# Kernel optimization log

Hardware: AMD Instinct MI355X
Metric: run time of the kernel (lower is better)

## Reference

```python
import jax, jax.numpy as jnp
import numpy as np

N_FFT = 512
N_STAGES = 4
BASE = N_FFT >> N_STAGES          # base DFT size = 32
SPLIT0 = N_FFT // 2 + 1           # rfft bins = 257
BATCH = 32768


def _mod_seq(order):
    # bit-reversed offset sequence used by get_partial_bit_reversal_matrix
    mset = [0]
    for o in range(order):
        step = 2 ** o
        mset = [v for x in mset for v in (x, x + step)]
    return mset


def _perm_indices():
    # gather indices equivalent to the partial bit-reversal permutation matmul
    base = 2 ** N_STAGES
    n_per = N_FFT // base
    idx = []
    for p in _mod_seq(N_STAGES):
        idx.extend(j * base + p for j in range(n_per))
    return np.asarray(idx, dtype=np.int32)

_PERM_IDX = _perm_indices()
_DFT = np.fft.fft(np.eye(BASE))   # symmetric DFT matrix, M[j,k]=exp(-2pi i jk/BASE)


def setup_inputs() -> dict:
    key = jax.random.key(0)
    x = jax.random.normal(key, (BATCH, N_FFT), dtype=jnp.float32)
    return {"x": x}


def reference(x):
    dt = x.dtype
    dft_r = jnp.asarray(_DFT.real, dtype=dt)
    dft_i = jnp.asarray(_DFT.imag, dtype=dt)

    B = x.shape[0]
    # partial bit-reversal permutation (FFTPermuter) as a gather
    y = x[..., _PERM_IDX].reshape(B, 2 ** N_STAGES, BASE)
    ev = y[:, ::2]   # even-decimated sub-sequences (B, 2^(s-1), BASE)
    od = y[:, 1::2]  # odd-decimated  sub-sequences

    # base-case DFT (DFT module): x @ M with symmetric M
    ev_r = jnp.einsum('bml,lk->bmk', ev, dft_r)
    ev_i = jnp.einsum('bml,lk->bmk', ev, dft_i)
    od_r = jnp.einsum('bml,lk->bmk', od, dft_r)
    od_i = jnp.einsum('bml,lk->bmk', od, dft_i)

    # radix-2 butterfly combine stages (FFTwiddle with SIMPLE ops)
    L = BASE
    for _ in range(N_STAGES):
        w = np.exp(-2j * np.pi * np.arange(L) / (2 * L))
        tw_r = jnp.asarray(w.real, dtype=dt)
        tw_i = jnp.asarray(w.imag, dtype=dt)
        todd_r = tw_r * od_r - tw_i * od_i
        todd_i = tw_r * od_i + tw_i * od_r
        real = jnp.concatenate([ev_r + todd_r, ev_r - todd_r], axis=-1)
        imag = jnp.concatenate([ev_i + todd_i, ev_i - todd_i], axis=-1)
        ev_r, od_r = real[:, ::2], real[:, 1::2]
        ev_i, od_i = imag[:, ::2], imag[:, 1::2]
        L *= 2

    # rfft truncation (torch.split in _RFFTDecompWithGMAC)
    yre = ev_r[:, 0, :SPLIT0]
    yim = ev_i[:, 0, :SPLIT0]
    return (yre, yim)
```

## Files before the change

kernel.cpp:

```cpp
#include <hip/hip_runtime.h>


#define NFFT 512
#define WPB  4

__device__ __forceinline__ int SW(int i) { return i ^ ((i >> 2) & 12); }

__device__ __forceinline__ void waveSyncLds() {
    asm volatile("s_waitcnt lgkmcnt(0)" ::: "memory");
}

__global__ __launch_bounds__(256) void rfft512_kernel(
    const float* __restrict__ x, float* __restrict__ out, int batch)
{
    __shared__ __align__(16) float2 lds[WPB][2][256];
    const int t = threadIdx.x & 63;
    const int w = threadIdx.x >> 6;
    long long b = (long long)blockIdx.x * WPB + w;
    if (b >= batch) b = batch - 1;

    float2* buf0 = lds[w][0];
    float2* buf1 = lds[w][1];
    const float NEG2PI = -6.28318530717958647692f;
    const float C45 = 0.70710678118654752440f;

    {
        const float2* xf2 = (const float2*)(x + b * NFFT);
        float2 a  = xf2[t];
        float2 bb = xf2[t + 64];
        float2 c  = xf2[t + 128];
        float2 d  = xf2[t + 192];
        float apcr = a.x + c.x, apci = a.y + c.y;
        float amcr = a.x - c.x, amci = a.y - c.y;
        float bpdr = bb.x + d.x, bpdi = bb.y + d.y;
        float bmdr = bb.x - d.x, bmdi = bb.y - d.y;
        float y0r = apcr + bpdr, y0i = apci + bpdi;
        float u1r = amcr + bmdi, u1i = amci - bmdr;
        float u2r = apcr - bpdr, u2i = apci - bpdi;
        float u3r = amcr - bmdi, u3i = amci + bmdr;
        float sn, cs;
        __sincosf(NEG2PI * (float)t * (1.0f / 256.0f), &sn, &cs);
        float w1r = cs, w1i = sn;
        float w2r = cs * cs - sn * sn, w2i = 2.0f * cs * sn;
        float w3r = w1r * w2r - w1i * w2i, w3i = w1r * w2i + w1i * w2r;
        int wb = (4 * t) ^ (t & 12);
        float4* d4 = (float4*)buf1;
        d4[wb >> 1]       = make_float4(y0r, y0i,
                                        w1r * u1r - w1i * u1i, w1r * u1i + w1i * u1r);
        d4[(wb >> 1) + 1] = make_float4(w2r * u2r - w2i * u2i, w2r * u2i + w2i * u2r,
                                        w3r * u3r - w3i * u3i, w3r * u3i + w3i * u3r);
    }
    waveSyncLds();

    {
        int rb = SW(t);
        float2 a = buf1[rb], bb = buf1[rb + 64], c = buf1[rb + 128], d = buf1[rb + 192];
        float apcr = a.x + c.x, apci = a.y + c.y;
        float amcr = a.x - c.x, amci = a.y - c.y;
        float bpdr = bb.x + d.x, bpdi = bb.y + d.y;
        float bmdr = bb.x - d.x, bmdi = bb.y - d.y;
        float y0r = apcr + bpdr, y0i = apci + bpdi;
        float u1r = amcr + bmdi, u1i = amci - bmdr;
        float u2r = apcr - bpdr, u2i = apci - bpdi;
        float u3r = amcr - bmdi, u3i = amci + bmdr;
        float sn, cs;
        __sincosf(NEG2PI * (float)(t >> 2) * (1.0f / 64.0f), &sn, &cs);
        float w1r = cs, w1i = sn;
        float w2r = cs * cs - sn * sn, w2i = 2.0f * cs * sn;
        float w3r = w1r * w2r - w1i * w2i, w3i = w1r * w2i + w1i * w2r;
        int wbase = (t & 3) + 16 * (t >> 2);
        buf0[SW(wbase)]      = make_float2(y0r, y0i);
        buf0[SW(wbase + 4)]  = make_float2(w1r * u1r - w1i * u1i, w1r * u1i + w1i * u1r);
        buf0[SW(wbase + 8)]  = make_float2(w2r * u2r - w2i * u2i, w2r * u2i + w2i * u2r);
        buf0[SW(wbase + 12)] = make_float2(w3r * u3r - w3i * u3i, w3r * u3i + w3i * u3r);
    }
    waveSyncLds();

    {
        int rb = SW(t);
        float2 a = buf0[rb], bb = buf0[rb + 64], c = buf0[rb + 128], d = buf0[rb + 192];
        float apcr = a.x + c.x, apci = a.y + c.y;
        float amcr = a.x - c.x, amci = a.y - c.y;
        float bpdr = bb.x + d.x, bpdi = bb.y + d.y;
        float bmdr = bb.x - d.x, bmdi = bb.y - d.y;
        float y0r = apcr + bpdr, y0i = apci + bpdi;
        float u1r = amcr + bmdi, u1i = amci - bmdr;
        float u2r = apcr - bpdr, u2i = apci - bpdi;
        float u3r = amcr - bmdi, u3i = amci + bmdr;
        float sn, cs;
        __sincosf(NEG2PI * (float)(t >> 4) * (1.0f / 16.0f), &sn, &cs);
        float w1r = cs, w1i = sn;
        float w2r = cs * cs - sn * sn, w2i = 2.0f * cs * sn;
        float w3r = w1r * w2r - w1i * w2i, w3i = w1r * w2i + w1i * w2r;
        int wbase = (t & 15) + 64 * (t >> 4);
        buf1[SW(wbase)]      = make_float2(y0r, y0i);
        buf1[SW(wbase + 16)] = make_float2(w1r * u1r - w1i * u1i, w1r * u1i + w1i * u1r);
        buf1[SW(wbase + 32)] = make_float2(w2r * u2r - w2i * u2i, w2r * u2i + w2i * u2r);
        buf1[SW(wbase + 48)] = make_float2(w3r * u3r - w3i * u3i, w3r * u3i + w3i * u3r);
    }
    waveSyncLds();

    float zr[4], zi[4];
    {
        int rb = SW(t);
        float2 a = buf1[rb], bb = buf1[rb + 64], c = buf1[rb + 128], d = buf1[rb + 192];
        float apcr = a.x + c.x, apci = a.y + c.y;
        float amcr = a.x - c.x, amci = a.y - c.y;
        float bpdr = bb.x + d.x, bpdi = bb.y + d.y;
        float bmdr = bb.x - d.x, bmdi = bb.y - d.y;
        zr[0] = apcr + bpdr; zi[0] = apci + bpdi;
        zr[1] = amcr + bmdi; zi[1] = amci - bmdr;
        zr[2] = apcr - bpdr; zi[2] = apci - bpdi;
        zr[3] = amcr - bmdi; zi[3] = amci + bmdr;
        buf0[rb]       = make_float2(zr[0], zi[0]);
        buf0[rb + 64]  = make_float2(zr[1], zi[1]);
        buf0[rb + 128] = make_float2(zr[2], zi[2]);
        buf0[rb + 192] = make_float2(zr[3], zi[3]);
    }
    waveSyncLds();

    float wr[4], wi[4];
    {
        float sn, cs;
        __sincosf(NEG2PI * (float)t * (1.0f / 512.0f), &sn, &cs);
        wr[0] = cs;              wi[0] = sn;
        wr[1] = C45 * (cs + sn); wi[1] = C45 * (sn - cs);
        wr[2] = sn;              wi[2] = -cs;
        wr[3] = C45 * (sn - cs); wi[3] = -C45 * (cs + sn);
    }
    float* outRe = out + b * 257;
    float* outIm = out + (long long)batch * 257 + b * 257;
#pragma unroll
    for (int j = 0; j < 4; ++j) {
        int k = t + 64 * j;
        int km = (256 - k) & 255;
        float2 pm = buf0[SW(km)];
        float S = zr[j] + pm.x;
        float T = zi[j] - pm.y;
        float U = zi[j] + pm.y;
        float V = zr[j] - pm.x;
        outRe[k] = 0.5f * (S + wr[j] * U + wi[j] * V);
        outIm[k] = 0.5f * (T - wr[j] * V + wi[j] * U);
    }
    if (t == 0) {
        outRe[256] = zr[0] - zi[0];
        outIm[256] = 0.0f;
    }
}

extern "C" void kernel_launch(void* const* d_in, const int* in_sizes, int n_in,
                              void* d_out, int out_size, void* d_ws, size_t ws_size,
                              hipStream_t stream)
{
    const float* x = (const float*)d_in[0];
    float* out = (float*)d_out;
    const int batch = in_sizes[0] / NFFT;
    const int grid = (batch + WPB - 1) / WPB;
    rfft512_kernel<<<grid, 256, 0, stream>>>(x, out, batch);
}
```

Baseline: 110.6 us.

## Process two rows per wave with upfront loads and vectorized staged output stores

Each wave now handles two FFT rows, issuing all global loads for both rows before computing so the second row's load latency overlaps the first row's work. The final output is staged through LDS and written with 4-wide unaligned vector stores instead of scalar strided stores. The batch-bound clamp was removed, so correctness relies on the batch being a multiple of eight. Register pressure rises from holding the second row's inputs.

```diff
diff --git a/kernel.cpp b/kernel.cpp
--- a/kernel.cpp
+++ b/kernel.cpp
@@ -3,6 +3,8 @@
 
 #define NFFT 512
 #define WPB  4
+
+typedef float f4u __attribute__((ext_vector_type(4), aligned(4)));
 
 __device__ __forceinline__ int SW(int i) { return i ^ ((i >> 2) & 12); }
 
@@ -16,108 +18,22 @@
     __shared__ __align__(16) float2 lds[WPB][2][256];
     const int t = threadIdx.x & 63;
     const int w = threadIdx.x >> 6;
-    long long b = (long long)blockIdx.x * WPB + w;
-    if (b >= batch) b = batch - 1;
+    const long long b0 = ((long long)blockIdx.x * WPB + w) * 2;
 
     float2* buf0 = lds[w][0];
     float2* buf1 = lds[w][1];
     const float NEG2PI = -6.28318530717958647692f;
     const float C45 = 0.70710678118654752440f;
 
-    {
-        const float2* xf2 = (const float2*)(x + b * NFFT);
-        float2 a  = xf2[t];
-        float2 bb = xf2[t + 64];
-        float2 c  = xf2[t + 128];
-        float2 d  = xf2[t + 192];
-        float apcr = a.x + c.x, apci = a.y + c.y;
-        float amcr = a.x - c.x, amci = a.y - c.y;
-        float bpdr = bb.x + d.x, bpdi = bb.y + d.y;
-        float bmdr = bb.x - d.x, bmdi = bb.y - d.y;
-        float y0r = apcr + bpdr, y0i = apci + bpdi;
-        float u1r = amcr + bmdi, u1i = amci - bmdr;
-        float u2r = apcr - bpdr, u2i = apci - bpdi;
-        float u3r = amcr - bmdi, u3i = amci + bmdr;
-        float sn, cs;
-        __sincosf(NEG2PI * (float)t * (1.0f / 256.0f), &sn, &cs);
-        float w1r = cs, w1i = sn;
-        float w2r = cs * cs - sn * sn, w2i = 2.0f * cs * sn;
-        float w3r = w1r * w2r - w1i * w2i, w3i = w1r * w2i + w1i * w2r;
-        int wb = (4 * t) ^ (t & 12);
-        float4* d4 = (float4*)buf1;
-        d4[wb >> 1]       = make_float4(y0r, y0i,
-                                        w1r * u1r - w1i * u1i, w1r * u1i + w1i * u1r);
-        d4[(wb >> 1) + 1] = make_float4(w2r * u2r - w2i * u2i, w2r * u2i + w2i * u2r,
-                                        w3r * u3r - w3i * u3i, w3r * u3i + w3i * u3r);
+    float2 L[2][4];
+#pragma unroll
+    for (int r = 0; r < 2; ++r) {
+        const float2* xf2 = (const float2*)(x + (b0 + r) * NFFT);
+        L[r][0] = xf2[t];
+        L[r][1] = xf2[t + 64];
+        L[r][2] = xf2[t + 128];
+        L[r][3] = xf2[t + 192];
     }
-    waveSyncLds();
-
-    {
-        int rb = SW(t);
-        float2 a = buf1[rb], bb = buf1[rb + 64], c = buf1[rb + 128], d = buf1[rb + 192];
-        float apcr = a.x + c.x, apci = a.y + c.y;
-        float amcr = a.x - c.x, amci = a.y - c.y;
-        float bpdr = bb.x + d.x, bpdi = bb.y + d.y;
-        float bmdr = bb.x - d.x, bmdi = bb.y - d.y;
-        float y0r = apcr + bpdr, y0i = apci + bpdi;
-        float u1r = amcr + bmdi, u1i = amci - bmdr;
-        float u2r = apcr - bpdr, u2i = apci - bpdi;
-        float u3r = amcr - bmdi, u3i = amci + bmdr;
-        float sn, cs;
-        __sincosf(NEG2PI * (float)(t >> 2) * (1.0f / 64.0f), &sn, &cs);
-        float w1r = cs, w1i = sn;
-        float w2r = cs * cs - sn * sn, w2i = 2.0f * cs * sn;
-        float w3r = w1r * w2r - w1i * w2i, w3i = w1r * w2i + w1i * w2r;
-        int wbase = (t & 3) + 16 * (t >> 2);
-        buf0[SW(wbase)]      = make_float2(y0r, y0i);
-        buf0[SW(wbase + 4)]  = make_float2(w1r * u1r - w1i * u1i, w1r * u1i + w1i * u1r);
-        buf0[SW(wbase + 8)]  = make_float2(w2r * u2r - w2i * u2i, w2r * u2i + w2i * u2r);
-        buf0[SW(wbase + 12)] = make_float2(w3r * u3r - w3i * u3i, w3r * u3i + w3i * u3r);
-    }
-    waveSyncLds();
-
-    {
-        int rb = SW(t);
-        float2 a = buf0[rb], bb = buf0[rb + 64], c = buf0[rb + 128], d = buf0[rb + 192];
-        float apcr = a.x + c.x, apci = a.y + c.y;
-        float amcr = a.x - c.x, amci = a.y - c.y;
-        float bpdr = bb.x + d.x, bpdi = bb.y + d.y;
-        float bmdr = bb.x - d.x, bmdi = bb.y - d.y;
-        float y0r = apcr + bpdr, y0i = apci + bpdi;
-        float u1r = amcr + bmdi, u1i = amci - bmdr;
-        float u2r = apcr - bpdr, u2i = apci - bpdi;
-        float u3r = amcr - bmdi, u3i = amci + bmdr;
-        float sn, cs;
-        __sincosf(NEG2PI * (float)(t >> 4) * (1.0f / 16.0f), &sn, &cs);
-        float w1r = cs, w1i = sn;
-        float w2r = cs * cs - sn * sn, w2i = 2.0f * cs * sn;
-        float w3r = w1r * w2r - w1i * w2i, w3i = w1r * w2i + w1i * w2r;
-        int wbase = (t & 15) + 64 * (t >> 4);
-        buf1[SW(wbase)]      = make_float2(y0r, y0i);
-        buf1[SW(wbase + 16)] = make_float2(w1r * u1r - w1i * u1i, w1r * u1i + w1i * u1r);
-        buf1[SW(wbase + 32)] = make_float2(w2r * u2r - w2i * u2i, w2r * u2i + w2i * u2r);
-        buf1[SW(wbase + 48)] = make_float2(w3r * u3r - w3i * u3i, w3r * u3i + w3i * u3r);
-    }
-    waveSyncLds();
-
-    float zr[4], zi[4];
-    {
-        int rb = SW(t);
-        float2 a = buf1[rb], bb = buf1[rb + 64], c = buf1[rb + 128], d = buf1[rb + 192];
-        float apcr = a.x + c.x, apci = a.y + c.y;
-        float amcr = a.x - c.x, amci = a.y - c.y;
-        float bpdr = bb.x + d.x, bpdi = bb.y + d.y;
-        float bmdr = bb.x - d.x, bmdi = bb.y - d.y;
-        zr[0] = apcr + bpdr; zi[0] = apci + bpdi;
-        zr[1] = amcr + bmdi; zi[1] = amci - bmdr;
-        zr[2] = apcr - bpdr; zi[2] = apci - bpdi;
-        zr[3] = amcr - bmdi; zi[3] = amci + bmdr;
-        buf0[rb]       = make_float2(zr[0], zi[0]);
-        buf0[rb + 64]  = make_float2(zr[1], zi[1]);
-        buf0[rb + 128] = make_float2(zr[2], zi[2]);
-        buf0[rb + 192] = make_float2(zr[3], zi[3]);
-    }
-    waveSyncLds();
 
     float wr[4], wi[4];
     {
@@ -128,23 +44,129 @@
         wr[2] = sn;              wi[2] = -cs;
         wr[3] = C45 * (sn - cs); wi[3] = -C45 * (cs + sn);
     }
-    float* outRe = out + b * 257;
-    float* outIm = out + (long long)batch * 257 + b * 257;
+
 #pragma unroll
-    for (int j = 0; j < 4; ++j) {
-        int k = t + 64 * j;
-        int km = (256 - k) & 255;
-        float2 pm = buf0[SW(km)];
-        float S = zr[j] + pm.x;
-        float T = zi[j] - pm.y;
-        float U = zi[j] + pm.y;
-        float V = zr[j] - pm.x;
-        outRe[k] = 0.5f * (S + wr[j] * U + wi[j] * V);
-        outIm[k] = 0.5f * (T - wr[j] * V + wi[j] * U);
-    }
-    if (t == 0) {
-        outRe[256] = zr[0] - zi[0];
-        outIm[256] = 0.0f;
+    for (int r = 0; r < 2; ++r) {
+        const long long b = b0 + r;
+
+        {
+            float2 a = L[r][0], bb = L[r][1], c = L[r][2], d = L[r][3];
+            float apcr = a.x + c.x, apci = a.y + c.y;
+            float amcr = a.x - c.x, amci = a.y - c.y;
+            float bpdr = bb.x + d.x, bpdi = bb.y + d.y;
+            float bmdr = bb.x - d.x, bmdi = bb.y - d.y;
+            float y0r = apcr + bpdr, y0i = apci + bpdi;
+            float u1r = amcr + bmdi, u1i = amci - bmdr;
+            float u2r = apcr - bpdr, u2i = apci - bpdi;
+            float u3r = amcr - bmdi, u3i = amci + bmdr;
+            float sn, cs;
+            __sincosf(NEG2PI * (float)t * (1.0f / 256.0f), &sn, &cs);
+            float w1r = cs, w1i = sn;
+            float w2r = cs * cs - sn * sn, w2i = 2.0f * cs * sn;
+            float w3r = w1r * w2r - w1i * w2i, w3i = w1r * w2i + w1i * w2r;
+            int wb = (4 * t) ^ (t & 12);
+            float4* d4 = (float4*)buf1;
+            d4[wb >> 1]       = make_float4(y0r, y0i,
+                                            w1r * u1r - w1i * u1i, w1r * u1i + w1i * u1r);
+            d4[(wb >> 1) + 1] = make_float4(w2r * u2r - w2i * u2i, w2r * u2i + w2i * u2r,
+                                            w3r * u3r - w3i * u3i, w3r * u3i + w3i * u3r);
+        }
+        waveSyncLds();
+
+        {
+            int rb = SW(t);
+            float2 a = buf1[rb], bb = buf1[rb + 64], c = buf1[rb + 128], d = buf1[rb + 192];
+            float apcr = a.x + c.x, apci = a.y + c.y;
+            float amcr = a.x - c.x, amci = a.y - c.y;
+            float bpdr = bb.x + d.x, bpdi = bb.y + d.y;
+            float bmdr = bb.x - d.x, bmdi = bb.y - d.y;
+            float y0r = apcr + bpdr, y0i = apci + bpdi;
+            float u1r = amcr + bmdi, u1i = amci - bmdr;
+            float u2r = apcr - bpdr, u2i = apci - bpdi;
+            float u3r = amcr - bmdi, u3i = amci + bmdr;
+            float sn, cs;
+            __sincosf(NEG2PI * (float)(t >> 2) * (1.0f / 64.0f), &sn, &cs);
+            float w1r = cs, w1i = sn;
+            float w2r = cs * cs - sn * sn, w2i = 2.0f * cs * sn;
+            float w3r = w1r * w2r - w1i * w2i, w3i = w1r * w2i + w1i * w2r;
+            int wbase = (t & 3) + 16 * (t >> 2);
+            buf0[SW(wbase)]      = make_float2(y0r, y0i);
+            buf0[SW(wbase + 4)]  = make_float2(w1r * u1r - w1i * u1i, w1r * u1i + w1i * u1r);
+            buf0[SW(wbase + 8)]  = make_float2(w2r * u2r - w2i * u2i, w2r * u2i + w2i * u2r);
+            buf0[SW(wbase + 12)] = make_float2(w3r * u3r - w3i * u3i, w3r * u3i + w3i * u3r);
+        }
+        waveSyncLds();
+
+        {
+            int rb = SW(t);
+            float2 a = buf0[rb], bb = buf0[rb + 64], c = buf0[rb + 128], d = buf0[rb + 192];
+            float apcr = a.x + c.x, apci = a.y + c.y;
+            float amcr = a.x - c.x, amci = a.y - c.y;
+            float bpdr = bb.x + d.x, bpdi = bb.y + d.y;
+            float bmdr = bb.x - d.x, bmdi = bb.y - d.y;
+            float y0r = apcr + bpdr, y0i = apci + bpdi;
+            float u1r = amcr + bmdi, u1i = amci - bmdr;
+            float u2r = apcr - bpdr, u2i = apci - bpdi;
+            float u3r = amcr - bmdi, u3i = amci + bmdr;
+            float sn, cs;
+            __sincosf(NEG2PI * (float)(t >> 4) * (1.0f / 16.0f), &sn, &cs);
+            float w1r = cs, w1i = sn;
+            float w2r = cs * cs - sn * sn, w2i = 2.0f * cs * sn;
+            float w3r = w1r * w2r - w1i * w2i, w3i = w1r * w2i + w1i * w2r;
+            int wbase = (t & 15) + 64 * (t >> 4);
+            buf1[SW(wbase)]      = make_float2(y0r, y0i);
+            buf1[SW(wbase + 16)] = make_float2(w1r * u1r - w1i * u1i, w1r * u1i + w1i * u1r);
+            buf1[SW(wbase + 32)] = make_float2(w2r * u2r - w2i * u2i, w2r * u2i + w2i * u2r);
+            buf1[SW(wbase + 48)] = make_float2(w3r * u3r - w3i * u3i, w3r * u3i + w3i * u3r);
+        }
+        waveSyncLds();
+
+        float zr[4], zi[4];
+        {
+            int rb = SW(t);
+            float2 a = buf1[rb], bb = buf1[rb + 64], c = buf1[rb + 128], d = buf1[rb + 192];
+            float apcr = a.x + c.x, apci = a.y + c.y;
+            float amcr = a.x - c.x, amci = a.y - c.y;
+            float bpdr = bb.x + d.x, bpdi = bb.y + d.y;
+            float bmdr = bb.x - d.x, bmdi = bb.y - d.y;
+            zr[0] = apcr + bpdr; zi[0] = apci + bpdi;
+            zr[1] = amcr + bmdi; zi[1] = amci - bmdr;
+            zr[2] = apcr - bpdr; zi[2] = apci - bpdi;
+            zr[3] = amcr - bmdi; zi[3] = amci + bmdr;
+            buf0[rb]       = make_float2(zr[0], zi[0]);
+            buf0[rb + 64]  = make_float2(zr[1], zi[1]);
+            buf0[rb + 128] = make_float2(zr[2], zi[2]);
+            buf0[rb + 192] = make_float2(zr[3], zi[3]);
+        }
+        waveSyncLds();
+
+        float* fre = (float*)buf1;
+        float* fim = fre + 256;
+#pragma unroll
+        for (int j = 0; j < 4; ++j) {
+            int k = t + 64 * j;
+            int km = (256 - k) & 255;
+            float2 pm = buf0[SW(km)];
+            float S = zr[j] + pm.x;
+            float T = zi[j] - pm.y;
+            float U = zi[j] + pm.y;
+            float V = zr[j] - pm.x;
+            fre[k] = 0.5f * (S + wr[j] * U + wi[j] * V);
+            fim[k] = 0.5f * (T - wr[j] * V + wi[j] * U);
+        }
+        waveSyncLds();
+
+        float* outRe = out + b * 257;
+        float* outIm = out + (long long)batch * 257 + b * 257;
+        float4 vRe = ((const float4*)fre)[t];
+        float4 vIm = ((const float4*)fim)[t];
+        *(f4u*)(outRe + 4 * t) = (f4u){vRe.x, vRe.y, vRe.z, vRe.w};
+        *(f4u*)(outIm + 4 * t) = (f4u){vIm.x, vIm.y, vIm.z, vIm.w};
+        if (t == 0) {
+            outRe[256] = zr[0] - zi[0];
+            outIm[256] = 0.0f;
+        }
+        waveSyncLds();
     }
 }
 
@@ -155,6 +177,6 @@
     const float* x = (const float*)d_in[0];
     float* out = (float*)d_out;
     const int batch = in_sizes[0] / NFFT;
-    const int grid = (batch + WPB - 1) / WPB;
+    const int grid = (batch + WPB * 2 - 1) / (WPB * 2);
     rfft512_kernel<<<grid, 256, 0, stream>>>(x, out, batch);
 }
```

Measured after the change: 111.4 us. No clear change (+0.7%).
